# Kernel tuning notes

Measured on AMD Instinct MI355X. Metric: run time of the kernel, lower is better.

The kernel has to match this reference:

```python
import jax, jax.numpy as jnp
import numpy as np

N = 50000      # nodes
E = 800000     # edges (avg degree 16)
HID = 64       # hidden_dim
NH = 4         # heads
HC = HID // NH # channels per head = 16
EMB = 8        # emb_dim
EDIM = 6       # edge_dim
SDIM = 6       # state_dim
FEAT = 7       # raw node feature width
NSENS = 3


def setup_inputs() -> dict:
    key = jax.random.key(0)
    k = jax.random.split(key, 32)
    s = 0.1
    p = {}
    p['x'] = jax.random.normal(k[0], (N, FEAT), jnp.float32)
    p['node_type'] = jax.random.randint(k[1], (N,), 0, 2)
    p['sensor_id'] = jax.random.randint(k[2], (N,), 0, NSENS + 1)
    p['edge_index'] = jax.random.randint(k[3], (2, E), 0, N)
    p['edge_attr'] = jax.random.normal(k[4], (E, EDIM), jnp.float32)
    p['hidden_state'] = jnp.zeros((N, HID), jnp.float32)
    # embeddings
    p['type_emb'] = jax.random.normal(k[5], (2, EMB)) * s
    p['sensor_emb'] = jax.random.normal(k[6], (NSENS + 1, EMB)) * s
    # encoder MLP
    p['enc_w1'] = jax.random.normal(k[7], (FEAT + 2 * EMB, HID)) * s
    p['enc_b1'] = jnp.zeros((HID,))
    p['enc_w2'] = jax.random.normal(k[8], (HID, HID)) * s
    p['enc_b2'] = jnp.zeros((HID,))
    # GATv2 layer 1 (lin_l, lin_r with bias; lin_edge no bias; att [NH,HC]; out bias)
    p['g1_wl'] = jax.random.normal(k[9], (HID, HID)) * s
    p['g1_bl'] = jnp.zeros((HID,))
    p['g1_wr'] = jax.random.normal(k[10], (HID, HID)) * s
    p['g1_br'] = jnp.zeros((HID,))
    p['g1_we'] = jax.random.normal(k[11], (EDIM, HID)) * s
    p['g1_att'] = jax.random.normal(k[12], (NH, HC)) * s
    p['g1_bias'] = jnp.zeros((HID,))
    # GATv2 layer 2
    p['g2_wl'] = jax.random.normal(k[13], (HID, HID)) * s
    p['g2_bl'] = jnp.zeros((HID,))
    p['g2_wr'] = jax.random.normal(k[14], (HID, HID)) * s
    p['g2_br'] = jnp.zeros((HID,))
    p['g2_we'] = jax.random.normal(k[15], (EDIM, HID)) * s
    p['g2_att'] = jax.random.normal(k[16], (NH, HC)) * s
    p['g2_bias'] = jnp.zeros((HID,))
    # GRUCell (torch layout transposed: [in, 3*hid], gate order r,z,n)
    p['gru_wih'] = jax.random.normal(k[17], (HID, 3 * HID)) * s
    p['gru_bih'] = jnp.zeros((3 * HID,))
    p['gru_whh'] = jax.random.normal(k[18], (HID, 3 * HID)) * s
    p['gru_bhh'] = jnp.zeros((3 * HID,))
    # decoder MLP
    p['dec_w1'] = jax.random.normal(k[19], (HID, HID)) * s
    p['dec_b1'] = jnp.zeros((HID,))
    p['dec_w2'] = jax.random.normal(k[20], (HID, SDIM + 1)) * s
    p['dec_b2'] = jnp.zeros((SDIM + 1,))
    return p


def _gatv2(h, src, dst, edge_attr, wl, bl, wr, br, we, att, bias):
    # PyG GATv2Conv, concat=True, negative_slope=0.2, edge_dim features
    xl = (h @ wl + bl).reshape(-1, NH, HC)  # source transform [N,H,C]
    xr = (h @ wr + br).reshape(-1, NH, HC)  # target transform [N,H,C]
    xe = (edge_attr @ we).reshape(-1, NH, HC)  # edge transform [E,H,C]
    m = jax.nn.leaky_relu(xl[src] + xr[dst] + xe, 0.2)  # [E,H,C]
    logits = jnp.einsum('ehc,hc->eh', m, att)  # [E,H]
    # scatter-softmax over incoming edges of each destination node
    mx = jax.ops.segment_max(logits, dst, num_segments=N)
    ex = jnp.exp(logits - mx[dst])
    den = jax.ops.segment_sum(ex, dst, num_segments=N)
    alpha = ex / (den[dst] + 1e-16)  # [E,H]
    out = jax.ops.segment_sum(xl[src] * alpha[:, :, None], dst, num_segments=N)
    return out.reshape(-1, NH * HC) + bias, alpha


def reference(x, node_type, sensor_id, edge_index, edge_attr, hidden_state,
              type_emb, sensor_emb, enc_w1, enc_b1, enc_w2, enc_b2,
              g1_wl, g1_bl, g1_wr, g1_br, g1_we, g1_att, g1_bias,
              g2_wl, g2_bl, g2_wr, g2_br, g2_we, g2_att, g2_bias,
              gru_wih, gru_bih, gru_whh, gru_bhh,
              dec_w1, dec_b1, dec_w2, dec_b2):
    src, dst = edge_index[0], edge_index[1]
    h = jnp.concatenate([x, type_emb[node_type], sensor_emb[sensor_id]], axis=-1)
    h = jax.nn.relu(h @ enc_w1 + enc_b1) @ enc_w2 + enc_b2
    h, alpha1 = _gatv2(h, src, dst, edge_attr, g1_wl, g1_bl, g1_wr, g1_br, g1_we, g1_att, g1_bias)
    h = jax.nn.relu(h)
    h, alpha2 = _gatv2(h, src, dst, edge_attr, g2_wl, g2_bl, g2_wr, g2_br, g2_we, g2_att, g2_bias)
    # GRUCell (torch gate order: r, z, n)
    gi = h @ gru_wih + gru_bih
    gh = hidden_state @ gru_whh + gru_bhh
    r = jax.nn.sigmoid(gi[:, :HID] + gh[:, :HID])
    z = jax.nn.sigmoid(gi[:, HID:2 * HID] + gh[:, HID:2 * HID])
    n = jnp.tanh(gi[:, 2 * HID:] + r * gh[:, 2 * HID:])
    new_hidden = (1.0 - z) * n + z * hidden_state
    out = jax.nn.relu(new_hidden @ dec_w1 + dec_b1) @ dec_w2 + dec_b2
    return out, new_hidden, alpha1, alpha2
```

## Files before the change

kernel.cpp:

```cpp
#include <hip/hip_runtime.h>
#include <hip/hip_bf16.h>

static constexpr int N_ = 50000;
static constexpr int E_ = 800000;
static constexpr int CAP = 128;


#define GEMM_FMA_BLOCK(AV, W0, W1, ROW)                                              \
      acc[ROW][0]=fmaf(AV,W0.x,acc[ROW][0]); acc[ROW][1]=fmaf(AV,W0.y,acc[ROW][1]);  \
      acc[ROW][2]=fmaf(AV,W0.z,acc[ROW][2]); acc[ROW][3]=fmaf(AV,W0.w,acc[ROW][3]);  \
      acc[ROW][4]=fmaf(AV,W1.x,acc[ROW][4]); acc[ROW][5]=fmaf(AV,W1.y,acc[ROW][5]);  \
      acc[ROW][6]=fmaf(AV,W1.z,acc[ROW][6]); acc[ROW][7]=fmaf(AV,W1.w,acc[ROW][7]);

#define GEMM_KLOOP(KQc)                                                              \
  _Pragma("unroll 1")                                                                \
  for (int kg = 0; kg < (KQc); ++kg) {                                               \
    float4 a0 = At4[kg * 129 + rowb];                                                \
    float4 a1 = At4[kg * 129 + rowb + 32];                                           \
    float4 a2 = At4[kg * 129 + rowb + 64];                                           \
    float4 a3 = At4[kg * 129 + rowb + 96];                                           \
    _Pragma("unroll")                                                                \
    for (int t = 0; t < 4; ++t) {                                                    \
      float4 w0 = *(const float4*)(Wt + (kg * 4 + t) * 64 + j0);                     \
      float4 w1 = *(const float4*)(Wt + (kg * 4 + t) * 64 + j0 + 4);                 \
      float av0 = t==0?a0.x:t==1?a0.y:t==2?a0.z:a0.w;                                \
      float av1 = t==0?a1.x:t==1?a1.y:t==2?a1.z:a1.w;                                \
      float av2 = t==0?a2.x:t==1?a2.y:t==2?a2.z:a2.w;                                \
      float av3 = t==0?a3.x:t==1?a3.y:t==2?a3.z:a3.w;                                \
      GEMM_FMA_BLOCK(av0, w0, w1, 0)                                                 \
      GEMM_FMA_BLOCK(av1, w0, w1, 1)                                                 \
      GEMM_FMA_BLOCK(av2, w0, w1, 2)                                                 \
      GEMM_FMA_BLOCK(av3, w0, w1, 3)                                                 \
    }                                                                                \
  }

#define ACC_INIT(BPTR)                                                               \
  {                                                                                  \
    float4 b0v = *(const float4*)((BPTR) + j0);                                      \
    float4 b1v = *(const float4*)((BPTR) + j0 + 4);                                  \
    _Pragma("unroll")                                                                \
    for (int i = 0; i < 4; ++i) {                                                    \
      acc[i][0]=b0v.x; acc[i][1]=b0v.y; acc[i][2]=b0v.z; acc[i][3]=b0v.w;            \
      acc[i][4]=b1v.x; acc[i][5]=b1v.y; acc[i][6]=b1v.z; acc[i][7]=b1v.w;            \
    }                                                                                \
  }

#define STAGE_W(WPTR, LDW, KPADc, KREAL)                                             \
  for (int idx = tid; idx < (KPADc) * 16; idx += 256) {                              \
    int k = idx >> 4, jq = idx & 15;                                                 \
    float4 v = (k < (KREAL)) ? *(const float4*)((WPTR) + (size_t)k * (LDW) + jq * 4) \
                             : make_float4(0.f, 0.f, 0.f, 0.f);                      \
    *(float4*)(Wt + k * 64 + jq * 4) = v;                                            \
  }

#define STAGE_A(APTR, LDA, KQc)                                                      \
  for (int idx = tid; idx < 128 * (KQc); idx += 256) {                               \
    int r = idx / (KQc), kq = idx - r * (KQc);                                       \
    int node = nb + r;                                                               \
    float4 v = (node < N_) ? *(const float4*)((APTR) + (size_t)node * (LDA) + kq * 4)\
                           : make_float4(0.f, 0.f, 0.f, 0.f);                        \
    At4[kq * 129 + r] = v;                                                           \
  }

#define STORE_C(CPTR, LDC, RELUc, ACCc)                                              \
  _Pragma("unroll")                                                                  \
  for (int i = 0; i < 4; ++i) {                                                      \
    int node = nb + rowb + 32 * i;                                                   \
    if (node < N_) {                                                                 \
      float* cp = (CPTR) + (size_t)node * (LDC) + j0;                                \
      float o0=acc[i][0],o1=acc[i][1],o2=acc[i][2],o3=acc[i][3];                     \
      float o4=acc[i][4],o5=acc[i][5],o6=acc[i][6],o7=acc[i][7];                     \
      if (RELUc) { o0=fmaxf(o0,0.f);o1=fmaxf(o1,0.f);o2=fmaxf(o2,0.f);o3=fmaxf(o3,0.f); \
                   o4=fmaxf(o4,0.f);o5=fmaxf(o5,0.f);o6=fmaxf(o6,0.f);o7=fmaxf(o7,0.f); } \
      if (ACCc) { float4 c0=*(const float4*)cp; float4 c1=*(const float4*)(cp+4);    \
                  o0+=c0.x;o1+=c0.y;o2+=c0.z;o3+=c0.w;o4+=c1.x;o5+=c1.y;o6+=c1.z;o7+=c1.w; } \
      *(float4*)cp = make_float4(o0,o1,o2,o3);                                       \
      *(float4*)(cp+4) = make_float4(o4,o5,o6,o7);                                   \
    }                                                                                \
  }

__global__ void k_hist(const int* __restrict__ ei, int* __restrict__ deg) {
  int e = blockIdx.x * blockDim.x + threadIdx.x;
  if (e < E_) atomicAdd(&deg[ei[E_ + e]], 1);
}

__global__ __launch_bounds__(1024) void k_scan_blk(const int* __restrict__ deg,
                                                   int* __restrict__ off,
                                                   int* __restrict__ bsum) {
  __shared__ int sm[1024];
  int t = threadIdx.x;
  int i = blockIdx.x * 1024 + t;
  int v = (i < N_) ? deg[i] : 0;
  sm[t] = v;
  __syncthreads();
  for (int s = 1; s < 1024; s <<= 1) {
    int u = (t >= s) ? sm[t - s] : 0;
    __syncthreads();
    sm[t] += u;
    __syncthreads();
  }
  if (i < N_) off[i] = sm[t] - v;
  if (t == 1023) bsum[blockIdx.x] = sm[t];
}

__global__ void k_scan_top(int* __restrict__ bsum, int nb) {
  int t = threadIdx.x;
  int v = (t < nb) ? bsum[t] : 0;
  int orig = v;
  for (int s = 1; s < 64; s <<= 1) {
    int u = __shfl_up(v, s);
    if (t >= s) v += u;
  }
  if (t < nb) bsum[t] = v - orig;
}

__global__ void k_scan_add(int* __restrict__ off, const int* __restrict__ bsum,
                           int* __restrict__ cur) {
  int i = blockIdx.x * blockDim.x + threadIdx.x;
  if (i < N_) {
    int o = off[i] + bsum[i >> 10];
    off[i] = o;
    cur[i] = o;
  }
  if (i == 0) off[N_] = E_;
}

__global__ void k_scatter(const int* __restrict__ ei, int* __restrict__ cursor,
                          int2* __restrict__ csr_es) {
  int e = blockIdx.x * blockDim.x + threadIdx.x;
  if (e < E_) {
    int s = ei[e];
    int d = ei[E_ + e];
    int p = atomicAdd(&cursor[d], 1);
    csr_es[p] = make_int2(e, s);
  }
}

__global__ void k_eaperm(const int2* __restrict__ csr_es, const float* __restrict__ eattr,
                         float4* __restrict__ eaA, float2* __restrict__ eaB) {
  int p = blockIdx.x * blockDim.x + threadIdx.x;
  if (p < E_) {
    int e = csr_es[p].x;
    const float* ep = eattr + (size_t)e * 6;
    eaA[p] = make_float4(ep[0], ep[1], ep[2], ep[3]);
    eaB[p] = make_float2(ep[4], ep[5]);
  }
}

__device__ __forceinline__ float encval(int c, int node, int nt, int sd,
                                        const float* __restrict__ x,
                                        const float* __restrict__ temb,
                                        const float* __restrict__ semb) {
  if (c < 7) return x[node * 7 + c];
  if (c < 15) return temb[nt * 8 + c - 7];
  if (c < 23) return semb[sd * 8 + c - 15];
  return 0.f;
}

__global__ __launch_bounds__(256, 3) void k_enc(
    const float* __restrict__ x, const int* __restrict__ ntype, const int* __restrict__ sid,
    const float* __restrict__ temb, const float* __restrict__ semb,
    const float* __restrict__ w1, const float* __restrict__ b1,
    const float* __restrict__ w2, const float* __restrict__ b2,
    float* __restrict__ hout) {
  __shared__ float4 At4[16 * 129];
  __shared__ float Wt[64 * 64];
  int tid = threadIdx.x;
  int nb = blockIdx.x * 128;
  for (int idx = tid; idx < 128 * 6; idx += 256) {
    int r = idx / 6, kq = idx - r * 6;
    int node = nb + r;
    float v0 = 0.f, v1 = 0.f, v2 = 0.f, v3 = 0.f;
    if (node < N_) {
      int nt = ntype[node], sd = sid[node];
      int c = kq * 4;
      v0 = encval(c, node, nt, sd, x, temb, semb);
      v1 = encval(c + 1, node, nt, sd, x, temb, semb);
      v2 = encval(c + 2, node, nt, sd, x, temb, semb);
      v3 = encval(c + 3, node, nt, sd, x, temb, semb);
    }
    At4[kq * 129 + r] = make_float4(v0, v1, v2, v3);
  }
  STAGE_W(w1, 64, 24, 23)
  __syncthreads();
  int col = tid & 7, rowb = tid >> 3;
  int j0 = col * 8;
  float acc[4][8];
  ACC_INIT(b1)
  GEMM_KLOOP(6)
  __syncthreads();
#pragma unroll
  for (int i = 0; i < 4; ++i) {
    int rl = rowb + 32 * i;
    At4[(col * 2) * 129 + rl] =
        make_float4(fmaxf(acc[i][0], 0.f), fmaxf(acc[i][1], 0.f),
                    fmaxf(acc[i][2], 0.f), fmaxf(acc[i][3], 0.f));
    At4[(col * 2 + 1) * 129 + rl] =
        make_float4(fmaxf(acc[i][4], 0.f), fmaxf(acc[i][5], 0.f),
                    fmaxf(acc[i][6], 0.f), fmaxf(acc[i][7], 0.f));
  }
  STAGE_W(w2, 64, 64, 64)
  __syncthreads();
  ACC_INIT(b2)
  GEMM_KLOOP(16)
  STORE_C(hout, 64, false, false)
}

__global__ __launch_bounds__(256, 3) void k_gemm2(
    const float* __restrict__ A,
    const float* __restrict__ Wl, const float* __restrict__ bl,
    const float* __restrict__ Wr, const float* __restrict__ br,
    float* __restrict__ Cl, float* __restrict__ Cr) {
  __shared__ float4 At4[16 * 129];
  __shared__ float Wt[64 * 64];
  int tid = threadIdx.x;
  int nb = blockIdx.x * 128;
  const float* W = blockIdx.y ? Wr : Wl;
  const float* b = blockIdx.y ? br : bl;
  float* C       = blockIdx.y ? Cr : Cl;
  STAGE_A(A, 64, 16)
  STAGE_W(W, 64, 64, 64)
  __syncthreads();
  int col = tid & 7, rowb = tid >> 3;
  int j0 = col * 8;
  float acc[4][8];
  ACC_INIT(b)
  GEMM_KLOOP(16)
  STORE_C(C, 64, false, false)
}

__global__ __launch_bounds__(256, 3) void k_gru(
    const float* __restrict__ hA, const float* __restrict__ hs,
    const float* __restrict__ wih, const float* __restrict__ bih,
    const float* __restrict__ whh, const float* __restrict__ bhh,
    float* __restrict__ outnh) {
  __shared__ float4 At4[16 * 129];
  __shared__ float Wt[64 * 64];
  int tid = threadIdx.x;
  int nb = blockIdx.x * 128;
  int col = tid & 7, rowb = tid >> 3;
  int j0 = col * 8;
  float g0[4][8], g1[4][8], g2[4][8];
  STAGE_A(hA, 64, 16)
  STAGE_W(wih + 0, 192, 64, 64)
  __syncthreads();
  { auto& acc = g0; ACC_INIT(bih + 0) GEMM_KLOOP(16) }
  __syncthreads();
  STAGE_W(wih + 64, 192, 64, 64)
  __syncthreads();
  { auto& acc = g1; ACC_INIT(bih + 64) GEMM_KLOOP(16) }
  __syncthreads();
  STAGE_W(wih + 128, 192, 64, 64)
  __syncthreads();
  { auto& acc = g2; ACC_INIT(bih + 128) GEMM_KLOOP(16) }
  __syncthreads();
  STAGE_A(hs, 64, 16)
  STAGE_W(whh + 0, 192, 64, 64)
  __syncthreads();
  float gh[4][8];
  { auto& acc = gh; ACC_INIT(bhh + 0) GEMM_KLOOP(16) }
#pragma unroll
  for (int i = 0; i < 4; ++i)
#pragma unroll
    for (int u = 0; u < 8; ++u)
      g0[i][u] = 1.f / (1.f + __expf(-(g0[i][u] + gh[i][u])));
  __syncthreads();
  STAGE_W(whh + 64, 192, 64, 64)
  __syncthreads();
  { auto& acc = gh; ACC_INIT(bhh + 64) GEMM_KLOOP(16) }
#pragma unroll
  for (int i = 0; i < 4; ++i)
#pragma unroll
    for (int u = 0; u < 8; ++u)
      g1[i][u] = 1.f / (1.f + __expf(-(g1[i][u] + gh[i][u])));
  __syncthreads();
  STAGE_W(whh + 128, 192, 64, 64)
  __syncthreads();
  { auto& acc = gh; ACC_INIT(bhh + 128) GEMM_KLOOP(16) }
#pragma unroll
  for (int i = 0; i < 4; ++i)
#pragma unroll
    for (int u = 0; u < 8; ++u)
      g2[i][u] = tanhf(g2[i][u] + g0[i][u] * gh[i][u]);
#pragma unroll
  for (int i = 0; i < 4; ++i) {
    int node = nb + rowb + 32 * i;
    if (node < N_) {
      int rl = rowb + 32 * i;
      float4 s0 = At4[(col * 2) * 129 + rl];
      float4 s1 = At4[(col * 2 + 1) * 129 + rl];
      float q0 = (1.f - g1[i][0]) * g2[i][0] + g1[i][0] * s0.x;
      float q1 = (1.f - g1[i][1]) * g2[i][1] + g1[i][1] * s0.y;
      float q2 = (1.f - g1[i][2]) * g2[i][2] + g1[i][2] * s0.z;
      float q3 = (1.f - g1[i][3]) * g2[i][3] + g1[i][3] * s0.w;
      float q4 = (1.f - g1[i][4]) * g2[i][4] + g1[i][4] * s1.x;
      float q5 = (1.f - g1[i][5]) * g2[i][5] + g1[i][5] * s1.y;
      float q6 = (1.f - g1[i][6]) * g2[i][6] + g1[i][6] * s1.z;
      float q7 = (1.f - g1[i][7]) * g2[i][7] + g1[i][7] * s1.w;
      float* op = outnh + (size_t)node * 64 + j0;
      *(float4*)op = make_float4(q0, q1, q2, q3);
      *(float4*)(op + 4) = make_float4(q4, q5, q6, q7);
    }
  }
}

__global__ __launch_bounds__(256, 3) void k_dec(
    const float* __restrict__ A,
    const float* __restrict__ w1, const float* __restrict__ b1,
    const float* __restrict__ w2, const float* __restrict__ b2,
    float* __restrict__ out) {
  __shared__ __align__(16) float pool[8320];
  __shared__ float Wt[64 * 64];
  float4* At4 = (float4*)pool;
  float* dtile = pool;
  int tid = threadIdx.x;
  int nb = blockIdx.x * 128;
  STAGE_A(A, 64, 16)
  STAGE_W(w1, 64, 64, 64)
  __syncthreads();
  int col = tid & 7, rowb = tid >> 3;
  int j0 = col * 8;
  float acc[4][8];
  ACC_INIT(b1)
  GEMM_KLOOP(16)
  __syncthreads();
#pragma unroll
  for (int i = 0; i < 4; ++i) {
    int rl = rowb + 32 * i;
#pragma unroll
    for (int u = 0; u < 8; ++u) dtile[rl * 65 + j0 + u] = fmaxf(acc[i][u], 0.f);
  }
  __syncthreads();
  if (tid < 128) {
    int node = nb + tid;
    if (node < N_) {
      float o0 = b2[0], o1 = b2[1], o2 = b2[2], o3 = b2[3], o4 = b2[4], o5 = b2[5], o6 = b2[6];
#pragma unroll 1
      for (int k = 0; k < 64; ++k) {
        float xv = dtile[tid * 65 + k];
        o0 = fmaf(xv, w2[k * 7 + 0], o0);
        o1 = fmaf(xv, w2[k * 7 + 1], o1);
        o2 = fmaf(xv, w2[k * 7 + 2], o2);
        o3 = fmaf(xv, w2[k * 7 + 3], o3);
        o4 = fmaf(xv, w2[k * 7 + 4], o4);
        o5 = fmaf(xv, w2[k * 7 + 5], o5);
        o6 = fmaf(xv, w2[k * 7 + 6], o6);
      }
      float* op = out + (size_t)node * 7;
      op[0] = o0; op[1] = o1; op[2] = o2; op[3] = o3; op[4] = o4; op[5] = o5; op[6] = o6;
    }
  }
}

template <bool RELU>
__global__ __launch_bounds__(64, 6) void k_fused(
    const int* __restrict__ off, const int2* __restrict__ csr_es,
    const float* __restrict__ eaA, const float* __restrict__ eaB,
    const float* __restrict__ xl, const float* __restrict__ xr,
    const float* __restrict__ we, const float* __restrict__ att,
    const float* __restrict__ bias,
    float* __restrict__ hout, float* __restrict__ alpha) {
  __shared__ float wes[6 * 64];
  __shared__ float exbuf[CAP * 4];
  __shared__ int ebuf[CAP];
  int lane = threadIdx.x & 63;
  int slot = lane >> 4;
  int q = lane & 15;
  int head = q >> 2;
  int sb = slot << 4;
  int v = blockIdx.x;

#pragma unroll
  for (int i = 0; i < 6; ++i) wes[i * 64 + lane] = we[i * 64 + lane];

  int p0 = off[v], p1 = off[v + 1];
  int cnt = p1 - p0;

  float att4[4], b4[4];
#pragma unroll
  for (int r = 0; r < 4; ++r) { att4[r] = att[q * 4 + r]; b4[r] = bias[q * 4 + r]; }

  float4 xr4 = *(const float4*)(xr + (size_t)v * 64 + q * 4);
  float num0 = 0.f, num1 = 0.f, num2 = 0.f, num3 = 0.f, den = 0.f;

  __syncthreads();

  int p = p0 + slot;
  int2 es = (p < p1) ? csr_es[p] : make_int2(0, 0);
  for (int base = 0; base < cnt; base += 4) {
    int pc = p0 + base + slot;
    bool valid = pc < p1;
    int e = es.x, s = es.y;
    int pn = pc + 4;
    int2 esn = (pn < p1) ? csr_es[pn] : make_int2(0, 0);
    float ea = 0.f;
    if (valid) {
      if (q < 4)      ea = eaA[(size_t)pc * 4 + q];
      else if (q < 6) ea = eaB[(size_t)pc * 2 + (q - 4)];
    }
    float4 xls = valid ? *(const float4*)(xl + (size_t)s * 64 + q * 4)
                       : make_float4(0.f, 0.f, 0.f, 0.f);
    float m0 = xls.x + xr4.x, m1 = xls.y + xr4.y, m2 = xls.z + xr4.z, m3 = xls.w + xr4.w;
#pragma unroll
    for (int i = 0; i < 6; ++i) {
      float eai = __shfl(ea, sb + i);
      float4 w4 = *(const float4*)(wes + i * 64 + q * 4);
      m0 = fmaf(eai, w4.x, m0);
      m1 = fmaf(eai, w4.y, m1);
      m2 = fmaf(eai, w4.z, m2);
      m3 = fmaf(eai, w4.w, m3);
    }
    m0 = (m0 > 0.f) ? m0 : 0.2f * m0;
    m1 = (m1 > 0.f) ? m1 : 0.2f * m1;
    m2 = (m2 > 0.f) ? m2 : 0.2f * m2;
    m3 = (m3 > 0.f) ? m3 : 0.2f * m3;
    float t = m0 * att4[0];
    t = fmaf(m1, att4[1], t);
    t = fmaf(m2, att4[2], t);
    t = fmaf(m3, att4[3], t);
    t += __shfl_xor(t, 1);
    t += __shfl_xor(t, 2);
    float ex = valid ? __expf(t) : 0.f;
    den += ex;
    num0 = fmaf(xls.x, ex, num0);
    num1 = fmaf(xls.y, ex, num1);
    num2 = fmaf(xls.z, ex, num2);
    num3 = fmaf(xls.w, ex, num3);
    int idx = base + slot;
    if (valid && idx < CAP) {
      if ((lane & 3) == 0) exbuf[idx * 4 + head] = ex;
      if (q == 0) ebuf[idx] = e;
    }
    es = esn;
  }
  num0 += __shfl_xor(num0, 16); num0 += __shfl_xor(num0, 32);
  num1 += __shfl_xor(num1, 16); num1 += __shfl_xor(num1, 32);
  num2 += __shfl_xor(num2, 16); num2 += __shfl_xor(num2, 32);
  num3 += __shfl_xor(num3, 16); num3 += __shfl_xor(num3, 32);
  den  += __shfl_xor(den, 16);  den  += __shfl_xor(den, 32);
  float dinv = 1.f / (den + 1e-16f);
  float o0 = fmaf(num0, dinv, b4[0]);
  float o1 = fmaf(num1, dinv, b4[1]);
  float o2 = fmaf(num2, dinv, b4[2]);
  float o3 = fmaf(num3, dinv, b4[3]);
  if (RELU) {
    o0 = fmaxf(o0, 0.f); o1 = fmaxf(o1, 0.f); o2 = fmaxf(o2, 0.f); o3 = fmaxf(o3, 0.f);
  }
  if (slot == 0)
    *(float4*)(hout + (size_t)v * 64 + q * 4) = make_float4(o0, o1, o2, o3);
  float dh = __shfl(dinv, (lane & 3) << 2);
  if (cnt <= CAP) {
    for (int base2 = 0; base2 < cnt; base2 += 16) {
      int idx = base2 + (lane >> 2);
      if (idx < cnt) {
        float exv = exbuf[idx * 4 + (lane & 3)];
        int e = ebuf[idx];
        alpha[(size_t)e * 4 + (lane & 3)] = exv * dh;
      }
    }
  } else {
    for (int pp = p0; pp < p1; ++pp) {
      int2 es2 = csr_es[pp];
      int e = es2.x, s = es2.y;
      float ea = 0.f;
      if (q < 4)      ea = eaA[(size_t)pp * 4 + q];
      else if (q < 6) ea = eaB[(size_t)pp * 2 + (q - 4)];
      float4 xls = *(const float4*)(xl + (size_t)s * 64 + q * 4);
      float m0 = xls.x + xr4.x, m1 = xls.y + xr4.y, m2 = xls.z + xr4.z, m3 = xls.w + xr4.w;
#pragma unroll
      for (int i = 0; i < 6; ++i) {
        float eai = __shfl(ea, i);
        float4 w4 = *(const float4*)(wes + i * 64 + q * 4);
        m0 = fmaf(eai, w4.x, m0);
        m1 = fmaf(eai, w4.y, m1);
        m2 = fmaf(eai, w4.z, m2);
        m3 = fmaf(eai, w4.w, m3);
      }
      m0 = (m0 > 0.f) ? m0 : 0.2f * m0;
      m1 = (m1 > 0.f) ? m1 : 0.2f * m1;
      m2 = (m2 > 0.f) ? m2 : 0.2f * m2;
      m3 = (m3 > 0.f) ? m3 : 0.2f * m3;
      float t = m0 * att4[0];
      t = fmaf(m1, att4[1], t);
      t = fmaf(m2, att4[2], t);
      t = fmaf(m3, att4[3], t);
      t += __shfl_xor(t, 1);
      t += __shfl_xor(t, 2);
      if (slot == 0 && (lane & 3) == 0)
        alpha[(size_t)e * 4 + head] = __expf(t) * dinv;
    }
  }
}

extern "C" void kernel_launch(void* const* d_in, const int* in_sizes, int n_in,
                              void* d_out, int out_size, void* d_ws, size_t ws_size,
                              hipStream_t stream) {
  const float* x      = (const float*)d_in[0];
  const int* ntype    = (const int*)d_in[1];
  const int* sid      = (const int*)d_in[2];
  const int* ei       = (const int*)d_in[3];
  const float* eattr  = (const float*)d_in[4];
  const float* hs     = (const float*)d_in[5];
  const float* temb   = (const float*)d_in[6];
  const float* semb   = (const float*)d_in[7];
  const float* enc_w1 = (const float*)d_in[8];
  const float* enc_b1 = (const float*)d_in[9];
  const float* enc_w2 = (const float*)d_in[10];
  const float* enc_b2 = (const float*)d_in[11];
  const float* g1_wl  = (const float*)d_in[12];
  const float* g1_bl  = (const float*)d_in[13];
  const float* g1_wr  = (const float*)d_in[14];
  const float* g1_br  = (const float*)d_in[15];
  const float* g1_we  = (const float*)d_in[16];
  const float* g1_att = (const float*)d_in[17];
  const float* g1_bias= (const float*)d_in[18];
  const float* g2_wl  = (const float*)d_in[19];
  const float* g2_bl  = (const float*)d_in[20];
  const float* g2_wr  = (const float*)d_in[21];
  const float* g2_br  = (const float*)d_in[22];
  const float* g2_we  = (const float*)d_in[23];
  const float* g2_att = (const float*)d_in[24];
  const float* g2_bias= (const float*)d_in[25];
  const float* gru_wih= (const float*)d_in[26];
  const float* gru_bih= (const float*)d_in[27];
  const float* gru_whh= (const float*)d_in[28];
  const float* gru_bhh= (const float*)d_in[29];
  const float* dec_w1 = (const float*)d_in[30];
  const float* dec_b1 = (const float*)d_in[31];
  const float* dec_w2 = (const float*)d_in[32];
  const float* dec_b2 = (const float*)d_in[33];

  float* ws = (float*)d_ws;
  float* hA = ws;
  float* hB = hA + N_ * 64;
  float* xl = hB + N_ * 64;
  float* xr = xl + N_ * 64;
  float* U  = xr + N_ * 64;
  int* deg  = (int*)(U + N_ * 64);
  int* off  = deg + N_;
  int* cur  = off + N_ + 1;
  int* bsum = cur + N_;
  int2* csr_es = (int2*)(bsum + 64);
  float2* eaB = (float2*)(csr_es + E_);

  float4* eaA = (float4*)U;

  float* out0  = (float*)d_out;
  float* outnh = out0 + N_ * 7;
  float* outa1 = outnh + N_ * 64;
  float* outa2 = outa1 + E_ * 4;

  const int NB_SCAN = (N_ + 1023) / 1024;
  const int NB_GEMM = (N_ + 127) / 128;

  hipMemsetAsync(deg, 0, N_ * sizeof(int), stream);
  k_hist<<<(E_ + 255) / 256, 256, 0, stream>>>(ei, deg);
  k_scan_blk<<<NB_SCAN, 1024, 0, stream>>>(deg, off, bsum);
  k_scan_top<<<1, 64, 0, stream>>>(bsum, NB_SCAN);
  k_scan_add<<<(N_ + 255) / 256, 256, 0, stream>>>(off, bsum, cur);
  k_scatter<<<(E_ + 255) / 256, 256, 0, stream>>>(ei, cur, csr_es);
  k_eaperm<<<(E_ + 255) / 256, 256, 0, stream>>>(csr_es, eattr, eaA, eaB);

  k_enc<<<NB_GEMM, 256, 0, stream>>>(x, ntype, sid, temb, semb,
                                     enc_w1, enc_b1, enc_w2, enc_b2, hA);
  k_gemm2<<<dim3(NB_GEMM, 2), 256, 0, stream>>>(hA, g1_wl, g1_bl, g1_wr, g1_br, xl, xr);
  k_fused<true><<<N_, 64, 0, stream>>>(off, csr_es, (const float*)eaA, (const float*)eaB,
                                       xl, xr, g1_we, g1_att, g1_bias, hB, outa1);
  k_gemm2<<<dim3(NB_GEMM, 2), 256, 0, stream>>>(hB, g2_wl, g2_bl, g2_wr, g2_br, xl, xr);
  k_fused<false><<<N_, 64, 0, stream>>>(off, csr_es, (const float*)eaA, (const float*)eaB,
                                        xl, xr, g2_we, g2_att, g2_bias, hA, outa2);
  k_gru<<<NB_GEMM, 256, 0, stream>>>(hA, hs, gru_wih, gru_bih, gru_whh, gru_bhh, outnh);
  k_dec<<<NB_GEMM, 256, 0, stream>>>(outnh, dec_w1, dec_b1, dec_w2, dec_b2, out0);
}
```

Baseline: 521.5 us.

## Write alpha via separate edge-order kernel using CSR position map

```diff
diff --git a/kernel.cpp b/kernel.cpp
--- a/kernel.cpp
+++ b/kernel.cpp
@@ -3,7 +3,6 @@
 
 static constexpr int N_ = 50000;
 static constexpr int E_ = 800000;
-static constexpr int CAP = 128;
 
 
 #define GEMM_FMA_BLOCK(AV, W0, W1, ROW)                                              \
@@ -126,13 +125,14 @@
 }
 
 __global__ void k_scatter(const int* __restrict__ ei, int* __restrict__ cursor,
-                          int2* __restrict__ csr_es) {
+                          int2* __restrict__ csr_es, int* __restrict__ pos) {
   int e = blockIdx.x * blockDim.x + threadIdx.x;
   if (e < E_) {
     int s = ei[e];
     int d = ei[E_ + e];
     int p = atomicAdd(&cursor[d], 1);
     csr_es[p] = make_int2(e, s);
+    pos[e] = p;
   }
 }
 
@@ -144,6 +144,20 @@
     const float* ep = eattr + (size_t)e * 6;
     eaA[p] = make_float4(ep[0], ep[1], ep[2], ep[3]);
     eaB[p] = make_float2(ep[4], ep[5]);
+  }
+}
+
+__global__ void k_alpha(const int* __restrict__ pos, const int* __restrict__ dei,
+                        const float* __restrict__ exP, const float* __restrict__ dinvN,
+                        float* __restrict__ alpha) {
+  int e = blockIdx.x * blockDim.x + threadIdx.x;
+  if (e < E_) {
+    int p = pos[e];
+    int d = dei[e];
+    float4 di = *(const float4*)(dinvN + (size_t)d * 4);
+    float4 x4 = *(const float4*)(exP + (size_t)p * 4);
+    *(float4*)(alpha + (size_t)e * 4) =
+        make_float4(x4.x * di.x, x4.y * di.y, x4.z * di.z, x4.w * di.w);
   }
 }
 
@@ -359,10 +373,8 @@
     const float* __restrict__ xl, const float* __restrict__ xr,
     const float* __restrict__ we, const float* __restrict__ att,
     const float* __restrict__ bias,
-    float* __restrict__ hout, float* __restrict__ alpha) {
+    float* __restrict__ hout, float* __restrict__ exP, float* __restrict__ dinvN) {
   __shared__ float wes[6 * 64];
-  __shared__ float exbuf[CAP * 4];
-  __shared__ int ebuf[CAP];
   int lane = threadIdx.x & 63;
   int slot = lane >> 4;
   int q = lane & 15;
@@ -390,7 +402,7 @@
   for (int base = 0; base < cnt; base += 4) {
     int pc = p0 + base + slot;
     bool valid = pc < p1;
-    int e = es.x, s = es.y;
+    int s = es.y;
     int pn = pc + 4;
     int2 esn = (pn < p1) ? csr_es[pn] : make_int2(0, 0);
     float ea = 0.f;
@@ -426,11 +438,7 @@
     num1 = fmaf(xls.y, ex, num1);
     num2 = fmaf(xls.z, ex, num2);
     num3 = fmaf(xls.w, ex, num3);
-    int idx = base + slot;
-    if (valid && idx < CAP) {
-      if ((lane & 3) == 0) exbuf[idx * 4 + head] = ex;
-      if (q == 0) ebuf[idx] = e;
-    }
+    if (valid && (lane & 3) == 0) exP[(size_t)pc * 4 + head] = ex;
     es = esn;
   }
   num0 += __shfl_xor(num0, 16); num0 += __shfl_xor(num0, 32);
@@ -448,48 +456,7 @@
   }
   if (slot == 0)
     *(float4*)(hout + (size_t)v * 64 + q * 4) = make_float4(o0, o1, o2, o3);
-  float dh = __shfl(dinv, (lane & 3) << 2);
-  if (cnt <= CAP) {
-    for (int base2 = 0; base2 < cnt; base2 += 16) {
-      int idx = base2 + (lane >> 2);
-      if (idx < cnt) {
-        float exv = exbuf[idx * 4 + (lane & 3)];
-        int e = ebuf[idx];
-        alpha[(size_t)e * 4 + (lane & 3)] = exv * dh;
-      }
-    }
-  } else {
-    for (int pp = p0; pp < p1; ++pp) {
-      int2 es2 = csr_es[pp];
-      int e = es2.x, s = es2.y;
-      float ea = 0.f;
-      if (q < 4)      ea = eaA[(size_t)pp * 4 + q];
-      else if (q < 6) ea = eaB[(size_t)pp * 2 + (q - 4)];
-      float4 xls = *(const float4*)(xl + (size_t)s * 64 + q * 4);
-      float m0 = xls.x + xr4.x, m1 = xls.y + xr4.y, m2 = xls.z + xr4.z, m3 = xls.w + xr4.w;
-#pragma unroll
-      for (int i = 0; i < 6; ++i) {
-        float eai = __shfl(ea, i);
-        float4 w4 = *(const float4*)(wes + i * 64 + q * 4);
-        m0 = fmaf(eai, w4.x, m0);
-        m1 = fmaf(eai, w4.y, m1);
-        m2 = fmaf(eai, w4.z, m2);
-        m3 = fmaf(eai, w4.w, m3);
-      }
-      m0 = (m0 > 0.f) ? m0 : 0.2f * m0;
-      m1 = (m1 > 0.f) ? m1 : 0.2f * m1;
-      m2 = (m2 > 0.f) ? m2 : 0.2f * m2;
-      m3 = (m3 > 0.f) ? m3 : 0.2f * m3;
-      float t = m0 * att4[0];
-      t = fmaf(m1, att4[1], t);
-      t = fmaf(m2, att4[2], t);
-      t = fmaf(m3, att4[3], t);
-      t += __shfl_xor(t, 1);
-      t += __shfl_xor(t, 2);
-      if (slot == 0 && (lane & 3) == 0)
-        alpha[(size_t)e * 4 + head] = __expf(t) * dinv;
-    }
-  }
+  if (slot == 0 && (lane & 3) == 0) dinvN[(size_t)v * 4 + head] = dinv;
 }
 
 extern "C" void kernel_launch(void* const* d_in, const int* in_sizes, int n_in,
@@ -542,8 +509,12 @@
   int* bsum = cur + N_;
   int2* csr_es = (int2*)(bsum + 64);
   float2* eaB = (float2*)(csr_es + E_);
+  float* exP  = (float*)(eaB + E_);
+  int* pos    = (int*)(exP + (size_t)E_ * 4);
+  float* dinvN = (float*)(pos + E_);
 
   float4* eaA = (float4*)U;
+  const int* dei = ei + E_;
 
   float* out0  = (float*)d_out;
   float* outnh = out0 + N_ * 7;
@@ -552,23 +523,26 @@
 
   const int NB_SCAN = (N_ + 1023) / 1024;
   const int NB_GEMM = (N_ + 127) / 128;
+  const int NB_E = (E_ + 255) / 256;
 
   hipMemsetAsync(deg, 0, N_ * sizeof(int), stream);
-  k_hist<<<(E_ + 255) / 256, 256, 0, stream>>>(ei, deg);
+  k_hist<<<NB_E, 256, 0, stream>>>(ei, deg);
   k_scan_blk<<<NB_SCAN, 1024, 0, stream>>>(deg, off, bsum);
   k_scan_top<<<1, 64, 0, stream>>>(bsum, NB_SCAN);
   k_scan_add<<<(N_ + 255) / 256, 256, 0, stream>>>(off, bsum, cur);
-  k_scatter<<<(E_ + 255) / 256, 256, 0, stream>>>(ei, cur, csr_es);
-  k_eaperm<<<(E_ + 255) / 256, 256, 0, stream>>>(csr_es, eattr, eaA, eaB);
+  k_scatter<<<NB_E, 256, 0, stream>>>(ei, cur, csr_es, pos);
+  k_eaperm<<<NB_E, 256, 0, stream>>>(csr_es, eattr, eaA, eaB);
 
   k_enc<<<NB_GEMM, 256, 0, stream>>>(x, ntype, sid, temb, semb,
                                      enc_w1, enc_b1, enc_w2, enc_b2, hA);
   k_gemm2<<<dim3(NB_GEMM, 2), 256, 0, stream>>>(hA, g1_wl, g1_bl, g1_wr, g1_br, xl, xr);
   k_fused<true><<<N_, 64, 0, stream>>>(off, csr_es, (const float*)eaA, (const float*)eaB,
-                                       xl, xr, g1_we, g1_att, g1_bias, hB, outa1);
+                                       xl, xr, g1_we, g1_att, g1_bias, hB, exP, dinvN);
+  k_alpha<<<NB_E, 256, 0, stream>>>(pos, dei, exP, dinvN, outa1);
   k_gemm2<<<dim3(NB_GEMM, 2), 256, 0, stream>>>(hB, g2_wl, g2_bl, g2_wr, g2_br, xl, xr);
   k_fused<false><<<N_, 64, 0, stream>>>(off, csr_es, (const float*)eaA, (const float*)eaB,
-                                        xl, xr, g2_we, g2_att, g2_bias, hA, outa2);
+                                        xl, xr, g2_we, g2_att, g2_bias, hA, exP, dinvN);
+  k_alpha<<<NB_E, 256, 0, stream>>>(pos, dei, exP, dinvN, outa2);
   k_gru<<<NB_GEMM, 256, 0, stream>>>(hA, hs, gru_wih, gru_bih, gru_whh, gru_bhh, outnh);
   k_dec<<<NB_GEMM, 256, 0, stream>>>(outnh, dec_w1, dec_b1, dec_w2, dec_b2, out0);
 }
```

New measurement: 556.2 us. 1.07x slower.
